# Optimization experiments

Measured on AMD Instinct MI355X. Metric: run time of the kernel, lower is better.

The kernel has to match this reference:

```python
import jax, jax.numpy as jnp
import numpy as np

B, S, H = 128, 512, 512  # batch, seq_len, hidden_units; feature dim is 2H = 1024
D = 2 * H


def setup_inputs() -> dict:
    key = jax.random.key(0)
    ks = jax.random.split(key, 8)
    scale = 1.0 / np.sqrt(D)
    return {
        "h_dec": jax.random.normal(ks[0], (1, B, H), jnp.float32),
        "c_dec": jax.random.normal(ks[1], (1, B, H), jnp.float32),
        "encoder_output": jax.random.normal(ks[2], (B, S, D), jnp.float32),
        "x_padding_masks": jnp.ones((B, S), jnp.float32),
        "coverage_vector": jax.random.uniform(ks[3], (B, S), jnp.float32),
        "Wh_w": jax.random.normal(ks[4], (D, D), jnp.float32) * scale,
        "Ws_w": jax.random.normal(ks[5], (D, D), jnp.float32) * scale,
        "Ws_b": jax.random.normal(ks[6], (D,), jnp.float32) * scale,
        "v_w": jax.random.normal(ks[7], (D,), jnp.float32) * scale,
        "wc_w": jax.random.normal(jax.random.fold_in(key, 99), (D,), jnp.float32) * scale,
    }


def reference(h_dec, c_dec, encoder_output, x_padding_masks, coverage_vector,
              Wh_w, Ws_w, Ws_b, v_w, wc_w):
    # s_t: concat(h, c) -> (B, 2H)
    s_t = jnp.concatenate([h_dec[0], c_dec[0]], axis=-1)  # (B, D)
    enc_feat = jnp.einsum('bsd,ed->bse', encoder_output, Wh_w)       # Wh(enc)
    dec_feat = s_t @ Ws_w.T + Ws_b                                    # (B, D)
    cov_feat = coverage_vector[:, :, None] * wc_w[None, None, :]      # w_c(cov)
    att_inputs = enc_feat + dec_feat[:, None, :] + cov_feat           # (B, S, D)
    score = jnp.tanh(att_inputs) @ v_w                                # (B, S)
    aw = jax.nn.softmax(score, axis=1) * x_padding_masks              # masked softmax
    aw = aw / jnp.sum(aw, axis=1, keepdims=True)                      # renormalize
    context_vector = jnp.einsum('bs,bsd->bd', aw, encoder_output)     # (B, D)
    new_coverage = coverage_vector + aw
    return context_vector, aw, new_coverage
```

## Files before the change

kernel.cpp:

```cpp
#include <hip/hip_runtime.h>
#include <hip/hip_bf16.h>
#include <cstdint>
#include <cstddef>


typedef __attribute__((ext_vector_type(8))) short bf16x8;
typedef __attribute__((ext_vector_type(4))) float f32x4;

#define GLOBAL_AS(p) ((const __attribute__((address_space(1))) unsigned int*)(p))
#define LDS_AS(p)    ((__attribute__((address_space(3))) unsigned int*)(p))

__device__ __forceinline__ short f2bf(float f) {
    union { float f; uint32_t u; } v; v.f = f;
    uint32_t u = v.u + 0x7fffu + ((v.u >> 16) & 1u);
    return (short)(u >> 16);
}

__device__ __forceinline__ float bf2f(short s) {
    union { uint32_t u; float f; } v; v.u = ((uint32_t)(uint16_t)s) << 16;
    return v.f;
}

__device__ __forceinline__ bf16x8 cvt8(float4 a, float4 b) {
    bf16x8 r;
    r[0] = f2bf(a.x); r[1] = f2bf(a.y); r[2] = f2bf(a.z); r[3] = f2bf(a.w);
    r[4] = f2bf(b.x); r[5] = f2bf(b.y); r[6] = f2bf(b.z); r[7] = f2bf(b.w);
    return r;
}

__device__ __forceinline__ float fast_tanh(float x) {
    x = fminf(10.f, fmaxf(-10.f, x));
    float e = __expf(2.f * x);
    return (e - 1.f) / (e + 1.f);
}

__global__ __launch_bounds__(256) void cvt_plus_dec(
    const float* __restrict__ enc, const float* __restrict__ Wh,
    short* __restrict__ enc_bf, short* __restrict__ Wh_bf,
    const float* __restrict__ hd, const float* __restrict__ cd,
    const float* __restrict__ Ws, float* __restrict__ dec_part)
{
    __shared__ __align__(16) short As[128 * 40];
    __shared__ __align__(16) short Bs[128 * 40];
    const int t = threadIdx.x;

    if (blockIdx.x < 33280) {
        size_t i = ((size_t)blockIdx.x * 256 + t) * 8;
        const float* src; short* dst; size_t off;
        const size_t NE = 67108864;
        if (i < NE) { src = enc; dst = enc_bf; off = i; }
        else        { src = Wh;  dst = Wh_bf;  off = i - NE; }
        float4 a = *(const float4*)(src + off);
        float4 b = *(const float4*)(src + off + 4);
        *(bf16x8*)(dst + off) = cvt8(a, b);
        return;
    }

    const int bid = blockIdx.x - 33280;
    const int bx = bid & 7;
    const int kc = bid >> 3;
    const int wv = t >> 6, lane = t & 63, q = lane >> 4, c = lane & 15;
    const int wm = wv & 1, wn = wv >> 1;
    const int ar = t >> 1, ah = t & 1;

    const float* abase = ((kc < 2) ? hd : cd) + (size_t)ar * 512 + (kc & 1) * 256 + ah * 16;
    const float* bbase = Ws + ((size_t)(bx * 128 + ar)) * 1024 + kc * 256 + ah * 16;
    short* awr = &As[ar * 40 + ah * 16];
    short* bwr = &Bs[ar * 40 + ah * 16];

    f32x4 acc[4][4];
#pragma unroll
    for (int i = 0; i < 4; ++i)
#pragma unroll
        for (int j = 0; j < 4; ++j) acc[i][j] = (f32x4){0.f, 0.f, 0.f, 0.f};

    for (int k0 = 0; k0 < 256; k0 += 32) {
        const float4* ap = (const float4*)(abase + k0);
        const float4* bp = (const float4*)(bbase + k0);
        float4 a0 = ap[0], a1 = ap[1], a2 = ap[2], a3 = ap[3];
        float4 b0 = bp[0], b1 = bp[1], b2 = bp[2], b3 = bp[3];
        *(bf16x8*)awr = cvt8(a0, a1);
        *(bf16x8*)(awr + 8) = cvt8(a2, a3);
        *(bf16x8*)bwr = cvt8(b0, b1);
        *(bf16x8*)(bwr + 8) = cvt8(b2, b3);
        __syncthreads();
        bf16x8 af[4], bf[4];
#pragma unroll
        for (int i = 0; i < 4; ++i) af[i] = *(const bf16x8*)&As[(wm * 64 + i * 16 + c) * 40 + q * 8];
#pragma unroll
        for (int j = 0; j < 4; ++j) bf[j] = *(const bf16x8*)&Bs[(wn * 64 + j * 16 + c) * 40 + q * 8];
#pragma unroll
        for (int i = 0; i < 4; ++i)
#pragma unroll
            for (int j = 0; j < 4; ++j)
                acc[i][j] = __builtin_amdgcn_mfma_f32_16x16x32_bf16(af[i], bf[j], acc[i][j], 0, 0, 0);
        __syncthreads();
    }

    const int n0 = bx * 128 + wn * 64;
    float* dp = dec_part + (size_t)kc * 131072;
#pragma unroll
    for (int i = 0; i < 4; ++i)
#pragma unroll
        for (int rr = 0; rr < 4; ++rr) {
            int bidx = wm * 64 + i * 16 + q * 4 + rr;
#pragma unroll
            for (int j = 0; j < 4; ++j)
                dp[(size_t)bidx * 1024 + n0 + j * 16 + c] = acc[i][j][rr];
        }
}

__global__ __launch_bounds__(256, 2) void attn_score_gemm5(
    const short* __restrict__ encb, const short* __restrict__ Whb,
    const float* __restrict__ dec_part, const float* __restrict__ Wsb,
    const float* __restrict__ cov,
    const float* __restrict__ wc_w, const float* __restrict__ v_w,
    float* __restrict__ p_part)
{
    __shared__ __align__(16) short As[2][256 * 32];
    __shared__ __align__(16) short Bs[2][128 * 32];
    const int t = threadIdx.x;
    const int lin = blockIdx.x;
    const int xcd = lin & 7;
    const int kk  = lin >> 3;
    const int bx  = kk & 7;
    const int my  = xcd * 32 + (kk >> 3);
    const int m0  = my * 256;
    const int b   = my >> 1;
    const int s0  = (my & 1) * 256;

    const int wv = t >> 6, lane = t & 63, q = lane >> 4, c = lane & 15;

    const int srow4 = lane >> 2;
    const int gg = (lane & 3) ^ ((srow4 ^ (srow4 >> 2)) & 3);

    const short* ag[4];
    int loA[4];
#pragma unroll
    for (int p = 0; p < 4; ++p) {
        int row = p * 64 + wv * 16 + srow4;
        ag[p] = encb + ((size_t)(m0 + row)) * 1024 + gg * 8;
        loA[p] = (p * 64 + wv * 16) * 32;
    }
    const short* bg[2];
    int loB[2];
#pragma unroll
    for (int r = 0; r < 2; ++r) {
        int row = r * 64 + wv * 16 + srow4;
        bg[r] = Whb + ((size_t)(bx * 128 + row)) * 1024 + gg * 8;
        loB[r] = (r * 64 + wv * 16) * 32;
    }

    const int qa = (q ^ ((c ^ (c >> 2)) & 3)) * 8;

    f32x4 acc[4][8];
#pragma unroll
    for (int i = 0; i < 4; ++i)
#pragma unroll
        for (int j = 0; j < 8; ++j) acc[i][j] = (f32x4){0.f, 0.f, 0.f, 0.f};

#pragma unroll
    for (int p = 0; p < 4; ++p)
        __builtin_amdgcn_global_load_lds(GLOBAL_AS(ag[p]), LDS_AS(&As[0][loA[p]]), 16, 0, 0);
#pragma unroll
    for (int r = 0; r < 2; ++r)
        __builtin_amdgcn_global_load_lds(GLOBAL_AS(bg[r]), LDS_AS(&Bs[0][loB[r]]), 16, 0, 0);
    __syncthreads();

    for (int k0 = 0; k0 < 32; ++k0) {
        const int cur = k0 & 1;
        if (k0 < 31) {
            const int nxt = cur ^ 1;
            const int kb = (k0 + 1) * 32;
#pragma unroll
            for (int p = 0; p < 4; ++p)
                __builtin_amdgcn_global_load_lds(GLOBAL_AS(ag[p] + kb), LDS_AS(&As[nxt][loA[p]]), 16, 0, 0);
#pragma unroll
            for (int r = 0; r < 2; ++r)
                __builtin_amdgcn_global_load_lds(GLOBAL_AS(bg[r] + kb), LDS_AS(&Bs[nxt][loB[r]]), 16, 0, 0);
        }
        bf16x8 af[4], bf[8];
#pragma unroll
        for (int i = 0; i < 4; ++i) af[i] = *(const bf16x8*)&As[cur][(wv * 64 + i * 16 + c) * 32 + qa];
#pragma unroll
        for (int j = 0; j < 8; ++j) bf[j] = *(const bf16x8*)&Bs[cur][(j * 16 + c) * 32 + qa];
#pragma unroll
        for (int i = 0; i < 4; ++i)
#pragma unroll
            for (int j = 0; j < 8; ++j)
                acc[i][j] = __builtin_amdgcn_mfma_f32_16x16x32_bf16(af[i], bf[j], acc[i][j], 0, 0, 0);
        __syncthreads();
    }

    const int n0 = bx * 128;
    float v_e[8], wc_e[8], dec_e[8];
#pragma unroll
    for (int j = 0; j < 8; ++j) {
        int e = n0 + j * 16 + c;
        v_e[j]  = v_w[e];
        wc_e[j] = wc_w[e];
        float d = Wsb[e];
#pragma unroll
        for (int p = 0; p < 4; ++p) d += dec_part[(size_t)p * 131072 + (size_t)b * 1024 + e];
        dec_e[j] = d;
    }
    const float* covb = cov + (size_t)b * 512;
    float* pp = p_part + (size_t)bx * 65536 + (size_t)b * 512;
#pragma unroll
    for (int i = 0; i < 4; ++i)
#pragma unroll
        for (int rr = 0; rr < 4; ++rr) {
            int s = s0 + wv * 64 + i * 16 + q * 4 + rr;
            float cs = covb[s];
            float p = 0.f;
#pragma unroll
            for (int j = 0; j < 8; ++j) {
                float att = acc[i][j][rr] + dec_e[j] + cs * wc_e[j];
                p += v_e[j] * fast_tanh(att);
            }
            p += __shfl_xor(p, 1);
            p += __shfl_xor(p, 2);
            p += __shfl_xor(p, 4);
            p += __shfl_xor(p, 8);
            if (c == 0) pp[s] = p;
        }
}

__global__ __launch_bounds__(256) void attn_score_gemm_fb(
    const float* __restrict__ enc, const short* __restrict__ Wh,
    const float* __restrict__ dec_feat, const float* __restrict__ cov,
    const float* __restrict__ wc_w, const float* __restrict__ v_w,
    float* __restrict__ p_part)
{
    __shared__ __align__(16) short As[128 * 40];
    __shared__ __align__(16) short Bs[128 * 40];
    const int t = threadIdx.x;
    const int bx = blockIdx.x;
    const int by = blockIdx.y;
    const int b  = by >> 2;
    const int s0 = (by & 3) * 128;

    const int wv = t >> 6, lane = t & 63, q = lane >> 4, c = lane & 15;
    const int wm = wv & 1, wn = wv >> 1;
    const int ar = t >> 1, ah = t & 1;

    const float* aptr = enc + ((size_t)(by * 128 + ar)) * 1024 + ah * 16;
    const short* bptr = Wh + ((size_t)(bx * 128 + ar)) * 1024 + ah * 16;
    short* awr = &As[ar * 40 + ah * 16];
    short* bwr = &Bs[ar * 40 + ah * 16];

    f32x4 acc[4][4];
#pragma unroll
    for (int i = 0; i < 4; ++i)
#pragma unroll
        for (int j = 0; j < 4; ++j) acc[i][j] = (f32x4){0.f, 0.f, 0.f, 0.f};

    for (int k0 = 0; k0 < 1024; k0 += 32) {
        const float4* ap = (const float4*)(aptr + k0);
        float4 a0 = ap[0], a1 = ap[1], a2 = ap[2], a3 = ap[3];
        bf16x8 bv0 = *(const bf16x8*)(bptr + k0);
        bf16x8 bv1 = *(const bf16x8*)(bptr + k0 + 8);
        *(bf16x8*)awr = cvt8(a0, a1);
        *(bf16x8*)(awr + 8) = cvt8(a2, a3);
        *(bf16x8*)bwr = bv0;
        *(bf16x8*)(bwr + 8) = bv1;
        __syncthreads();
        bf16x8 af[4], bf[4];
#pragma unroll
        for (int i = 0; i < 4; ++i) af[i] = *(const bf16x8*)&As[(wm * 64 + i * 16 + c) * 40 + q * 8];
#pragma unroll
        for (int j = 0; j < 4; ++j) bf[j] = *(const bf16x8*)&Bs[(wn * 64 + j * 16 + c) * 40 + q * 8];
#pragma unroll
        for (int i = 0; i < 4; ++i)
#pragma unroll
            for (int j = 0; j < 4; ++j)
                acc[i][j] = __builtin_amdgcn_mfma_f32_16x16x32_bf16(af[i], bf[j], acc[i][j], 0, 0, 0);
        __syncthreads();
    }

    const int n0 = bx * 128 + wn * 64;
    float v_e[4], wc_e[4], dec_e[4];
#pragma unroll
    for (int j = 0; j < 4; ++j) {
        int e = n0 + j * 16 + c;
        v_e[j]  = v_w[e];
        wc_e[j] = wc_w[e];
        dec_e[j] = dec_feat[(size_t)b * 1024 + e];
    }
    const float* covb = cov + (size_t)b * 512;
    float* pp = p_part + ((size_t)(bx * 2 + wn)) * 65536 + (size_t)b * 512;
#pragma unroll
    for (int i = 0; i < 4; ++i)
#pragma unroll
        for (int rr = 0; rr < 4; ++rr) {
            int s = s0 + wm * 64 + i * 16 + q * 4 + rr;
            float cs = covb[s];
            float p = 0.f;
#pragma unroll
            for (int j = 0; j < 4; ++j) {
                float att = acc[i][j][rr] + dec_e[j] + cs * wc_e[j];
                p += v_e[j] * fast_tanh(att);
            }
            p += __shfl_xor(p, 1);
            p += __shfl_xor(p, 2);
            p += __shfl_xor(p, 4);
            p += __shfl_xor(p, 8);
            if (c == 0) pp[s] = p;
        }
}

__global__ __launch_bounds__(256) void dec_gemm(
    const float* __restrict__ hd, const float* __restrict__ cd,
    const short* __restrict__ Ws, const float* __restrict__ Wsb,
    float* __restrict__ dec_feat)
{
    __shared__ __align__(16) short As[128 * 40];
    __shared__ __align__(16) short Bs[128 * 40];
    const int t = threadIdx.x;
    const int bx = blockIdx.x;
    const int wv = t >> 6, lane = t & 63, q = lane >> 4, c = lane & 15;
    const int wm = wv & 1, wn = wv >> 1;
    const int ar = t >> 1, ah = t & 1;

    const short* bptr = Ws + ((size_t)(bx * 128 + ar)) * 1024 + ah * 16;
    short* awr = &As[ar * 40 + ah * 16];
    short* bwr = &Bs[ar * 40 + ah * 16];

    f32x4 acc[4][4];
#pragma unroll
    for (int i = 0; i < 4; ++i)
#pragma unroll
        for (int j = 0; j < 4; ++j) acc[i][j] = (f32x4){0.f, 0.f, 0.f, 0.f};

    for (int k0 = 0; k0 < 1024; k0 += 32) {
        const int k = k0 + ah * 16;
        const float* src = (k < 512) ? (hd + (size_t)ar * 512 + k)
                                     : (cd + (size_t)ar * 512 + (k - 512));
        const float4* ap = (const float4*)src;
        float4 a0 = ap[0], a1 = ap[1], a2 = ap[2], a3 = ap[3];
        bf16x8 bv0 = *(const bf16x8*)(bptr + k0);
        bf16x8 bv1 = *(const bf16x8*)(bptr + k0 + 8);
        *(bf16x8*)awr = cvt8(a0, a1);
        *(bf16x8*)(awr + 8) = cvt8(a2, a3);
        *(bf16x8*)bwr = bv0;
        *(bf16x8*)(bwr + 8) = bv1;
        __syncthreads();
        bf16x8 af[4], bf[4];
#pragma unroll
        for (int i = 0; i < 4; ++i) af[i] = *(const bf16x8*)&As[(wm * 64 + i * 16 + c) * 40 + q * 8];
#pragma unroll
        for (int j = 0; j < 4; ++j) bf[j] = *(const bf16x8*)&Bs[(wn * 64 + j * 16 + c) * 40 + q * 8];
#pragma unroll
        for (int i = 0; i < 4; ++i)
#pragma unroll
            for (int j = 0; j < 4; ++j)
                acc[i][j] = __builtin_amdgcn_mfma_f32_16x16x32_bf16(af[i], bf[j], acc[i][j], 0, 0, 0);
        __syncthreads();
    }

    const int n0 = bx * 128 + wn * 64;
    float wsb_e[4];
#pragma unroll
    for (int j = 0; j < 4; ++j) wsb_e[j] = Wsb[n0 + j * 16 + c];
#pragma unroll
    for (int i = 0; i < 4; ++i)
#pragma unroll
        for (int rr = 0; rr < 4; ++rr) {
            int bidx = wm * 64 + i * 16 + q * 4 + rr;
#pragma unroll
            for (int j = 0; j < 4; ++j) {
                int e = n0 + j * 16 + c;
                dec_feat[(size_t)bidx * 1024 + e] = acc[i][j][rr] + wsb_e[j];
            }
        }
}

__global__ __launch_bounds__(512) void softmax_kernel(
    const float* __restrict__ p_part, int ns, const float* __restrict__ mask,
    const float* __restrict__ cov, float* __restrict__ aw, float* __restrict__ ncov)
{
    __shared__ float red[8];
    const int b = blockIdx.x, t = threadIdx.x;
    const int w = t >> 6, lane = t & 63;
    const size_t idx = (size_t)b * 512 + t;

    float sc = 0.f;
    for (int k = 0; k < ns; ++k) sc += p_part[(size_t)k * 65536 + idx];

    float m = sc;
#pragma unroll
    for (int o = 1; o < 64; o <<= 1) m = fmaxf(m, __shfl_xor(m, o));
    if (lane == 0) red[w] = m;
    __syncthreads();
#pragma unroll
    for (int i = 0; i < 8; ++i) m = fmaxf(m, red[i]);
    __syncthreads();

    float e = __expf(sc - m);
    float s = e;
#pragma unroll
    for (int o = 1; o < 64; o <<= 1) s += __shfl_xor(s, o);
    if (lane == 0) red[w] = s;
    __syncthreads();
    s = 0.f;
#pragma unroll
    for (int i = 0; i < 8; ++i) s += red[i];
    __syncthreads();

    float wv = (e / s) * mask[idx];
    float s2 = wv;
#pragma unroll
    for (int o = 1; o < 64; o <<= 1) s2 += __shfl_xor(s2, o);
    if (lane == 0) red[w] = s2;
    __syncthreads();
    s2 = 0.f;
#pragma unroll
    for (int i = 0; i < 8; ++i) s2 += red[i];

    float awv = wv / s2;
    aw[idx] = awv;
    ncov[idx] = cov[idx] + awv;
}

__global__ __launch_bounds__(256) void context_part(
    const short* __restrict__ encb, const float* __restrict__ aw, float* __restrict__ cpart)
{
    const int sc = blockIdx.x & 7;
    const int b  = blockIdx.x >> 3;
    const int t  = threadIdx.x;
    const int dl = t & 127;
    const int si = t >> 7;
    const short* ebase = encb + ((size_t)(b * 512 + sc * 64 + si)) * 1024 + dl * 8;
    const float* awp = aw + (size_t)b * 512 + sc * 64 + si;
    float acc[8];
#pragma unroll
    for (int i = 0; i < 8; ++i) acc[i] = 0.f;
#pragma unroll 16
    for (int s = 0; s < 64; s += 2) {
        float w = awp[s];
        bf16x8 e = *(const bf16x8*)(ebase + (size_t)s * 1024);
#pragma unroll
        for (int i = 0; i < 8; ++i) acc[i] += w * bf2f(e[i]);
    }
    float* cp = cpart + ((size_t)(sc * 2 + si) * 128 + b) * 1024 + dl * 8;
    *(float4*)(cp)     = (float4){acc[0], acc[1], acc[2], acc[3]};
    *(float4*)(cp + 4) = (float4){acc[4], acc[5], acc[6], acc[7]};
}

__global__ __launch_bounds__(256) void ctx_reduce(
    const float* __restrict__ cpart, float* __restrict__ ctx)
{
    int i = blockIdx.x * 256 + threadIdx.x;
    float s = 0.f;
#pragma unroll
    for (int k = 0; k < 16; ++k) s += cpart[(size_t)k * 131072 + i];
    ctx[i] = s;
}

__global__ __launch_bounds__(256) void context_f32(
    const float* __restrict__ enc, const float* __restrict__ aw, float* __restrict__ ctx)
{
    const int schunk = blockIdx.x;
    const int b = blockIdx.y;
    const int t = threadIdx.x;
    const float* ebase = enc + ((size_t)(b * 512 + schunk * 128)) * 1024 + t * 4;
    const float* awp = aw + (size_t)b * 512 + schunk * 128;
    float ax = 0.f, ay = 0.f, az = 0.f, aww = 0.f;
#pragma unroll 4
    for (int s = 0; s < 128; ++s) {
        float w = awp[s];
        float4 e4 = *(const float4*)(ebase + (size_t)s * 1024);
        ax += w * e4.x; ay += w * e4.y; az += w * e4.z; aww += w * e4.w;
    }
    float* cp = ctx + (size_t)b * 1024 + t * 4;
    atomicAdd(cp + 0, ax);
    atomicAdd(cp + 1, ay);
    atomicAdd(cp + 2, az);
    atomicAdd(cp + 3, aww);
}

__global__ void cvt_f32_bf16(const float* __restrict__ src, short* __restrict__ dst, int n) {
    int i = (blockIdx.x * 256 + threadIdx.x) * 4;
    if (i < n) {
        float4 f = *(const float4*)(src + i);
        short4 o;
        o.x = f2bf(f.x); o.y = f2bf(f.y); o.z = f2bf(f.z); o.w = f2bf(f.w);
        *(short4*)(dst + i) = o;
    }
}

extern "C" void kernel_launch(void* const* d_in, const int* in_sizes, int n_in,
                              void* d_out, int out_size, void* d_ws, size_t ws_size,
                              hipStream_t stream) {
    const float* hd   = (const float*)d_in[0];
    const float* cd   = (const float*)d_in[1];
    const float* enc  = (const float*)d_in[2];
    const float* mask = (const float*)d_in[3];
    const float* cov  = (const float*)d_in[4];
    const float* Wh   = (const float*)d_in[5];
    const float* Ws   = (const float*)d_in[6];
    const float* Wsb  = (const float*)d_in[7];
    const float* vw   = (const float*)d_in[8];
    const float* wcw  = (const float*)d_in[9];

    float* out  = (float*)d_out;
    float* ctx  = out;
    float* aw   = out + 131072;
    float* ncov = out + 196608;

    char* ws = (char*)d_ws;
    float* p_part   = (float*)ws;
    float* dec_part = (float*)(ws + (2u << 20));
    short* Wh_bf    = (short*)(ws + (4u << 20));
    short* enc_bf   = (short*)(ws + (8u << 20));
    float* cpart    = (float*)ws;
    const size_t need_big = (8ull << 20) + (128ull << 20);

    if (ws_size >= need_big) {
        cvt_plus_dec<<<33312, 256, 0, stream>>>(enc, Wh, enc_bf, Wh_bf, hd, cd, Ws, dec_part);
        attn_score_gemm5<<<2048, 256, 0, stream>>>(enc_bf, Wh_bf, dec_part, Wsb, cov, wcw, vw, p_part);
        softmax_kernel<<<128, 512, 0, stream>>>(p_part, 8, mask, cov, aw, ncov);
        context_part<<<1024, 256, 0, stream>>>(enc_bf, aw, cpart);
        ctx_reduce<<<512, 256, 0, stream>>>(cpart, ctx);
    } else {
        float* p_part16 = (float*)ws;
        float* dec_feat = (float*)(ws + (4u << 20));
        short* Wh_bf2   = (short*)(ws + (4u << 20) + (512u << 10));
        short* Ws_bf    = (short*)(ws + (6u << 20) + (512u << 10));
        hipMemsetAsync(ctx, 0, 128 * 1024 * sizeof(float), stream);
        cvt_f32_bf16<<<1024, 256, 0, stream>>>(Wh, Wh_bf2, 1024 * 1024);
        cvt_f32_bf16<<<1024, 256, 0, stream>>>(Ws, Ws_bf, 1024 * 1024);
        dec_gemm<<<8, 256, 0, stream>>>(hd, cd, Ws_bf, Wsb, dec_feat);
        attn_score_gemm_fb<<<dim3(8, 512), 256, 0, stream>>>(enc, Wh_bf2, dec_feat, cov, wcw, vw, p_part16);
        softmax_kernel<<<128, 512, 0, stream>>>(p_part16, 16, mask, cov, aw, ncov);
        context_f32<<<dim3(4, 128), 256, 0, stream>>>(enc, aw, ctx);
    }
}
```

Baseline: 639.5 us.

## Rework score GEMM into 256x256 tiles with 8 waves and 4-stage LDS pipeline

Replaces the 256x128-tile, 4-wave score GEMM with a 256x256-tile, 8-wave kernel that splits each 64-wide K step into interleaved half-loads, barriers and priority-raised MFMA bursts. The aim is more data reuse per LDS byte and better overlap of global-to-LDS copies with MFMA work. The epilogue now writes 16 partial score slices per column group, so softmax reduces 16 partials, and the workspace is rearranged to fit the larger p_part buffer. Tanh is computed with a reciprocal-based form without clamping, which changes numerics slightly and relies on the exp saturating correctly for large inputs.

```diff
diff --git a/kernel.cpp b/kernel.cpp
--- a/kernel.cpp
+++ b/kernel.cpp
@@ -32,6 +32,11 @@
     x = fminf(10.f, fmaxf(-10.f, x));
     float e = __expf(2.f * x);
     return (e - 1.f) / (e + 1.f);
+}
+
+__device__ __forceinline__ float fast_tanh2(float x) {
+    float e = __expf(2.f * x);
+    return 1.f - 2.f * __builtin_amdgcn_rcpf(e + 1.f);
 }
 
 __global__ __launch_bounds__(256) void cvt_plus_dec(
@@ -110,93 +115,154 @@
         }
 }
 
-__global__ __launch_bounds__(256, 2) void attn_score_gemm5(
+
+#define BARRIER() do { asm volatile("" ::: "memory"); \
+    __builtin_amdgcn_s_barrier(); asm volatile("" ::: "memory"); } while (0)
+#define WAIT_LGKM0() do { asm volatile("s_waitcnt lgkmcnt(0)" ::: "memory"); \
+    __builtin_amdgcn_sched_barrier(0); } while (0)
+#define STAGE(gp, kcol, arr, bufks, a) \
+    __builtin_amdgcn_global_load_lds(GLOBAL_AS((gp) + (kcol)), \
+        LDS_AS(&(arr)[(bufks) * 8192 + (a) * 4096 + wst]), 16, 0, 0)
+
+__global__ __launch_bounds__(512, 2) void attn_score_gemm8(
     const short* __restrict__ encb, const short* __restrict__ Whb,
     const float* __restrict__ dec_part, const float* __restrict__ Wsb,
     const float* __restrict__ cov,
     const float* __restrict__ wc_w, const float* __restrict__ v_w,
     float* __restrict__ p_part)
 {
-    __shared__ __align__(16) short As[2][256 * 32];
-    __shared__ __align__(16) short Bs[2][128 * 32];
-    const int t = threadIdx.x;
+    __shared__ __align__(16) short SA[32768];
+    __shared__ __align__(16) short SB[32768];
+
+    const int tid = threadIdx.x;
+    const int wv = tid >> 6, lane = tid & 63, q = lane >> 4, c = lane & 15;
+    const int wm = wv >> 2, wn = wv & 3;
+
     const int lin = blockIdx.x;
     const int xcd = lin & 7;
-    const int kk  = lin >> 3;
-    const int bx  = kk & 7;
-    const int my  = xcd * 32 + (kk >> 3);
+    const int idx = lin >> 3;
+    const int bx  = idx & 3;
+    const int my  = xcd * 32 + (idx >> 2);
     const int m0  = my * 256;
+    const int n0  = bx * 256;
     const int b   = my >> 1;
-    const int s0  = (my & 1) * 256;
-
-    const int wv = t >> 6, lane = t & 63, q = lane >> 4, c = lane & 15;
-
-    const int srow4 = lane >> 2;
-    const int gg = (lane & 3) ^ ((srow4 ^ (srow4 >> 2)) & 3);
-
-    const short* ag[4];
-    int loA[4];
-#pragma unroll
-    for (int p = 0; p < 4; ++p) {
-        int row = p * 64 + wv * 16 + srow4;
-        ag[p] = encb + ((size_t)(m0 + row)) * 1024 + gg * 8;
-        loA[p] = (p * 64 + wv * 16) * 32;
-    }
-    const short* bg[2];
-    int loB[2];
-#pragma unroll
-    for (int r = 0; r < 2; ++r) {
-        int row = r * 64 + wv * 16 + srow4;
-        bg[r] = Whb + ((size_t)(bx * 128 + row)) * 1024 + gg * 8;
-        loB[r] = (r * 64 + wv * 16) * 32;
-    }
-
-    const int qa = (q ^ ((c ^ (c >> 2)) & 3)) * 8;
-
-    f32x4 acc[4][8];
-#pragma unroll
-    for (int i = 0; i < 4; ++i)
-#pragma unroll
-        for (int j = 0; j < 8; ++j) acc[i][j] = (f32x4){0.f, 0.f, 0.f, 0.f};
-
-#pragma unroll
-    for (int p = 0; p < 4; ++p)
-        __builtin_amdgcn_global_load_lds(GLOBAL_AS(ag[p]), LDS_AS(&As[0][loA[p]]), 16, 0, 0);
-#pragma unroll
-    for (int r = 0; r < 2; ++r)
-        __builtin_amdgcn_global_load_lds(GLOBAL_AS(bg[r]), LDS_AS(&Bs[0][loB[r]]), 16, 0, 0);
-    __syncthreads();
-
-    for (int k0 = 0; k0 < 32; ++k0) {
-        const int cur = k0 & 1;
-        if (k0 < 31) {
-            const int nxt = cur ^ 1;
-            const int kb = (k0 + 1) * 32;
-#pragma unroll
-            for (int p = 0; p < 4; ++p)
-                __builtin_amdgcn_global_load_lds(GLOBAL_AS(ag[p] + kb), LDS_AS(&As[nxt][loA[p]]), 16, 0, 0);
-#pragma unroll
-            for (int r = 0; r < 2; ++r)
-                __builtin_amdgcn_global_load_lds(GLOBAL_AS(bg[r] + kb), LDS_AS(&Bs[nxt][loB[r]]), 16, 0, 0);
-        }
-        bf16x8 af[4], bf[8];
-#pragma unroll
-        for (int i = 0; i < 4; ++i) af[i] = *(const bf16x8*)&As[cur][(wv * 64 + i * 16 + c) * 32 + qa];
-#pragma unroll
-        for (int j = 0; j < 8; ++j) bf[j] = *(const bf16x8*)&Bs[cur][(j * 16 + c) * 32 + qa];
+    const int s0c = (my & 1) * 256;
+
+    const int srow = tid >> 2;
+    const int SLOT = ((tid & 3) ^ ((tid >> 3) & 3)) * 8;
+    const short* gA0 = encb + (size_t)(m0 + srow) * 1024 + SLOT;
+    const short* gA1 = gA0 + 131072;
+    const short* gB0 = Whb + (size_t)(n0 + srow) * 1024 + SLOT;
+    const short* gB1 = gB0 + 131072;
+    const int wst = wv * 512;
+
+    const int sq = (q ^ ((c >> 1) & 3)) * 8;
+    int aoff[8], boff[4];
+#pragma unroll
+    for (int i = 0; i < 8; ++i) aoff[i] = (wm * 128 + i * 16 + c) * 32 + sq;
+#pragma unroll
+    for (int j = 0; j < 4; ++j) boff[j] = (wn * 64 + j * 16 + c) * 32 + sq;
+
+    f32x4 acc[8][4];
+#pragma unroll
+    for (int i = 0; i < 8; ++i)
+#pragma unroll
+        for (int j = 0; j < 4; ++j) acc[i][j] = (f32x4){0.f, 0.f, 0.f, 0.f};
+
+    STAGE(gA0,  0, SA, 0, 0);  STAGE(gA1,  0, SA, 0, 1);
+    STAGE(gB0,  0, SB, 0, 0);  STAGE(gB1,  0, SB, 0, 1);
+    STAGE(gA0, 32, SA, 1, 0);  STAGE(gA1, 32, SA, 1, 1);
+    STAGE(gB0, 32, SB, 1, 0);  STAGE(gB1, 32, SB, 1, 1);
+    STAGE(gA0, 64, SA, 2, 0);  STAGE(gA1, 64, SA, 2, 1);
+    STAGE(gB0, 64, SB, 2, 0);  STAGE(gB1, 64, SB, 2, 1);
+    asm volatile("s_waitcnt vmcnt(4)" ::: "memory");
+    __builtin_amdgcn_s_barrier();
+    asm volatile("" ::: "memory");
+
+#pragma unroll 2
+    for (int t = 0; t < 16; ++t) {
+        const int cur = t & 1, nxt = cur ^ 1;
+        const int kc = t * 64;
+        const short* A0 = &SA[cur * 16384];
+        const short* A1 = A0 + 8192;
+        const short* B0 = &SB[cur * 16384];
+        const short* B1 = B0 + 8192;
+
+        bf16x8 af[4], bfr[4];
+
+#pragma unroll
+        for (int i = 0; i < 4; ++i) af[i] = *(const bf16x8*)&A0[aoff[i]];
+#pragma unroll
+        for (int j = 0; j < 4; ++j) bfr[j] = *(const bf16x8*)&B0[boff[j]];
+        if (t < 15) { STAGE(gA0, kc + 96, SA, nxt * 2 + 1, 0);
+                      STAGE(gA1, kc + 96, SA, nxt * 2 + 1, 1); }
+        BARRIER();
+        WAIT_LGKM0();
+        __builtin_amdgcn_s_setprio(1);
 #pragma unroll
         for (int i = 0; i < 4; ++i)
 #pragma unroll
-            for (int j = 0; j < 8; ++j)
-                acc[i][j] = __builtin_amdgcn_mfma_f32_16x16x32_bf16(af[i], bf[j], acc[i][j], 0, 0, 0);
-        __syncthreads();
-    }
-
-    const int n0 = bx * 128;
-    float v_e[8], wc_e[8], dec_e[8];
-#pragma unroll
-    for (int j = 0; j < 8; ++j) {
-        int e = n0 + j * 16 + c;
+            for (int j = 0; j < 4; ++j)
+                acc[i][j] = __builtin_amdgcn_mfma_f32_16x16x32_bf16(af[i], bfr[j], acc[i][j], 0, 0, 0);
+        __builtin_amdgcn_s_setprio(0);
+        BARRIER();
+
+#pragma unroll
+        for (int i = 0; i < 4; ++i) af[i] = *(const bf16x8*)&A0[aoff[4 + i]];
+        if (t < 15) { STAGE(gB0, kc + 96, SB, nxt * 2 + 1, 0);
+                      STAGE(gB1, kc + 96, SB, nxt * 2 + 1, 1); }
+        BARRIER();
+        WAIT_LGKM0();
+        __builtin_amdgcn_s_setprio(1);
+#pragma unroll
+        for (int i = 0; i < 4; ++i)
+#pragma unroll
+            for (int j = 0; j < 4; ++j)
+                acc[4 + i][j] = __builtin_amdgcn_mfma_f32_16x16x32_bf16(af[i], bfr[j], acc[4 + i][j], 0, 0, 0);
+        __builtin_amdgcn_s_setprio(0);
+        BARRIER();
+
+#pragma unroll
+        for (int i = 0; i < 4; ++i) af[i] = *(const bf16x8*)&A1[aoff[i]];
+#pragma unroll
+        for (int j = 0; j < 4; ++j) bfr[j] = *(const bf16x8*)&B1[boff[j]];
+        if (t < 14) { STAGE(gA0, kc + 128, SA, cur * 2, 0);
+                      STAGE(gA1, kc + 128, SA, cur * 2, 1); }
+        BARRIER();
+        WAIT_LGKM0();
+        __builtin_amdgcn_s_setprio(1);
+#pragma unroll
+        for (int i = 0; i < 4; ++i)
+#pragma unroll
+            for (int j = 0; j < 4; ++j)
+                acc[i][j] = __builtin_amdgcn_mfma_f32_16x16x32_bf16(af[i], bfr[j], acc[i][j], 0, 0, 0);
+        __builtin_amdgcn_s_setprio(0);
+        BARRIER();
+
+#pragma unroll
+        for (int i = 0; i < 4; ++i) af[i] = *(const bf16x8*)&A1[aoff[4 + i]];
+        if (t < 14) { STAGE(gB0, kc + 128, SB, cur * 2, 0);
+                      STAGE(gB1, kc + 128, SB, cur * 2, 1); }
+        BARRIER();
+        WAIT_LGKM0();
+        __builtin_amdgcn_s_setprio(1);
+#pragma unroll
+        for (int i = 0; i < 4; ++i)
+#pragma unroll
+            for (int j = 0; j < 4; ++j)
+                acc[4 + i][j] = __builtin_amdgcn_mfma_f32_16x16x32_bf16(af[i], bfr[j], acc[4 + i][j], 0, 0, 0);
+        __builtin_amdgcn_s_setprio(0);
+        if (t <= 13) asm volatile("s_waitcnt vmcnt(4)" ::: "memory");
+        else         asm volatile("s_waitcnt vmcnt(0)" ::: "memory");
+        __builtin_amdgcn_s_barrier();
+        asm volatile("" ::: "memory");
+    }
+
+    const int eb = n0 + wn * 64;
+    float v_e[4], wc_e[4], dec_e[4];
+#pragma unroll
+    for (int j = 0; j < 4; ++j) {
+        int e = eb + j * 16 + c;
         v_e[j]  = v_w[e];
         wc_e[j] = wc_w[e];
         float d = Wsb[e];
@@ -204,25 +270,25 @@
         for (int p = 0; p < 4; ++p) d += dec_part[(size_t)p * 131072 + (size_t)b * 1024 + e];
         dec_e[j] = d;
     }
-    const float* covb = cov + (size_t)b * 512;
-    float* pp = p_part + (size_t)bx * 65536 + (size_t)b * 512;
-#pragma unroll
-    for (int i = 0; i < 4; ++i)
+    const float* covb = cov + (size_t)b * 512 + s0c;
+    float* pp = p_part + (size_t)(bx * 4 + wn) * 65536 + (size_t)my * 256;
+#pragma unroll
+    for (int i = 0; i < 8; ++i)
 #pragma unroll
         for (int rr = 0; rr < 4; ++rr) {
-            int s = s0 + wv * 64 + i * 16 + q * 4 + rr;
-            float cs = covb[s];
+            int r = wm * 128 + i * 16 + q * 4 + rr;
+            float cs = covb[r];
             float p = 0.f;
 #pragma unroll
-            for (int j = 0; j < 8; ++j) {
+            for (int j = 0; j < 4; ++j) {
                 float att = acc[i][j][rr] + dec_e[j] + cs * wc_e[j];
-                p += v_e[j] * fast_tanh(att);
+                p += v_e[j] * fast_tanh2(att);
             }
             p += __shfl_xor(p, 1);
             p += __shfl_xor(p, 2);
             p += __shfl_xor(p, 4);
             p += __shfl_xor(p, 8);
-            if (c == 0) pp[s] = p;
+            if (c == 0) pp[r] = p;
         }
 }
 
@@ -510,16 +576,16 @@
 
     char* ws = (char*)d_ws;
     float* p_part   = (float*)ws;
-    float* dec_part = (float*)(ws + (2u << 20));
-    short* Wh_bf    = (short*)(ws + (4u << 20));
+    float* dec_part = (float*)(ws + (4u << 20));
+    short* Wh_bf    = (short*)(ws + (6u << 20));
     short* enc_bf   = (short*)(ws + (8u << 20));
     float* cpart    = (float*)ws;
     const size_t need_big = (8ull << 20) + (128ull << 20);
 
     if (ws_size >= need_big) {
         cvt_plus_dec<<<33312, 256, 0, stream>>>(enc, Wh, enc_bf, Wh_bf, hd, cd, Ws, dec_part);
-        attn_score_gemm5<<<2048, 256, 0, stream>>>(enc_bf, Wh_bf, dec_part, Wsb, cov, wcw, vw, p_part);
-        softmax_kernel<<<128, 512, 0, stream>>>(p_part, 8, mask, cov, aw, ncov);
+        attn_score_gemm8<<<1024, 512, 0, stream>>>(enc_bf, Wh_bf, dec_part, Wsb, cov, wcw, vw, p_part);
+        softmax_kernel<<<128, 512, 0, stream>>>(p_part, 16, mask, cov, aw, ncov);
         context_part<<<1024, 256, 0, stream>>>(enc_bf, aw, cpart);
         ctx_reduce<<<512, 256, 0, stream>>>(cpart, ctx);
     } else {
```

New measurement: 589.3 us. -7.8%, faster.
